# Performance work log

Hardware: AMD Instinct MI355X
Metric: run time of the kernel (lower is better)

The kernel has to match this reference:

```python
import jax, jax.numpy as jnp
import numpy as np

N_ATOMS = 3
HIDDEN = 256
N_PAIRS = N_ATOMS * (N_ATOMS - 1) // 2  # 3
BATCH = 500000


def setup_inputs() -> dict:
    key = jax.random.key(0)
    ks = jax.random.split(key, 8)
    s1 = 1.0 / np.sqrt(N_PAIRS)
    s2 = 1.0 / np.sqrt(HIDDEN)
    return {
        "x": jax.random.normal(ks[0], (BATCH, N_ATOMS * 3), dtype=jnp.float32),
        "W1": jax.random.normal(ks[1], (N_PAIRS, HIDDEN), dtype=jnp.float32) * s1,
        "b1": jnp.zeros((HIDDEN,), dtype=jnp.float32),
        "W2": jax.random.normal(ks[2], (HIDDEN, HIDDEN), dtype=jnp.float32) * s2,
        "b2": jnp.zeros((HIDDEN,), dtype=jnp.float32),
        "W3": jax.random.normal(ks[3], (HIDDEN, 3), dtype=jnp.float32) * s2,
        "b3": jnp.zeros((3,), dtype=jnp.float32),
    }


def reference(x, W1, b1, W2, b2, W3, b3):
    # --- pairwise bond lengths (vectorized over batch) ---
    pts = x.reshape(-1, N_ATOMS, 3)                       # [B, n_atoms, 3]
    iu, ju = np.triu_indices(N_ATOMS, 1)                  # static index arrays
    diff = pts[:, iu, :] - pts[:, ju, :]                  # [B, n_pairs, 3]
    r = jnp.sqrt(jnp.sum(diff * diff, axis=-1))           # [B, n_pairs]
    # --- MLP: Dense->relu->Dense->relu->Dense (sizes=[256,256,3]) ---
    h = jax.nn.relu(r @ W1 + b1)                          # [B, 256]
    h = jax.nn.relu(h @ W2 + b2)                          # [B, 256]
    w = h @ W3 + b3                                       # [B, 3] -> (w00, w11, w01)
    # --- analytic eigenvalues of symmetric 2x2 [[w00,w01],[w01,w11]] ---
    # eigh returns ascending order: mean -/+ radius
    m = 0.5 * (w[:, 0] + w[:, 1])
    d = 0.5 * (w[:, 0] - w[:, 1])
    rad = jnp.sqrt(d * d + w[:, 2] * w[:, 2])
    return jnp.stack([m - rad, m + rad], axis=-1)         # [B, 2]
```

## Files before the change

### kernel.cpp

```cpp
#include <hip/hip_runtime.h>
#include <hip/hip_bf16.h>
#include <stdint.h>

typedef __attribute__((ext_vector_type(8))) short short8;
typedef __attribute__((ext_vector_type(4))) float f32x4;

#define NCHUNK 15625
#define NBLK 256
#define NTHR 512
#define NWAVE_TOT (NBLK * 8)

__device__ __forceinline__ unsigned short f2bf(float f) {
    unsigned int u = __float_as_uint(f);
    u = (u + 0x7fffu + ((u >> 16) & 1u)) >> 16;
    return (unsigned short)u;
}

__global__ void prep_kernel(const float* __restrict__ W1, const float* __restrict__ b1,
                            const float* __restrict__ W2, const float* __restrict__ b2,
                            const float* __restrict__ W3,
                            uint4* __restrict__ w2p, float4* __restrict__ w1b1,
                            float4* __restrict__ w3b2) {
    int id = blockIdx.x * 256 + threadIdx.x;
    if (id < 8192) {
        int lane = id & 63;
        int f = id >> 6;
        int s = f >> 4, t = f & 15;
        int g = lane >> 4, c = lane & 15;
        int n = t * 16 + c;
        int kbase = s * 32 + g * 8;
        unsigned int w[4];
#pragma unroll
        for (int jj = 0; jj < 4; ++jj) {
            unsigned int lo = f2bf(W2[(kbase + 2 * jj) * 256 + n]);
            unsigned int hi = f2bf(W2[(kbase + 2 * jj + 1) * 256 + n]);
            w[jj] = lo | (hi << 16);
        }
        w2p[id] = make_uint4(w[0], w[1], w[2], w[3]);
    } else if (id < 8448) {
        int k = id - 8192;
        w1b1[k] = make_float4(W1[k], W1[256 + k], W1[512 + k], b1[k]);
    } else if (id < 8704) {
        int c2 = id - 8448;
        w3b2[c2] = make_float4(W3[c2 * 3 + 0], W3[c2 * 3 + 1], W3[c2 * 3 + 2], b2[c2]);
    }
}

__global__ __launch_bounds__(NTHR, 2) void fused_kernel(
    const float* __restrict__ x, const uint4* __restrict__ w2p,
    const float4* __restrict__ w1b1, const float4* __restrict__ w3b2,
    const float* __restrict__ b3, float* __restrict__ out)
{
    extern __shared__ char smem[];
    const int tid = threadIdx.x;
    const int lane = tid & 63;
    const int g = lane >> 4;
    const int lr = lane & 15;

    {
        uint4* ls = (uint4*)smem;
#pragma unroll
        for (int it = 0; it < 16; ++it) {
            int idx = it * NTHR + tid;
            ls[idx] = w2p[idx];
        }
    }
    __syncthreads();

    const float b30 = b3[0], b31 = b3[1], b32 = b3[2];
    const short8* bfr = (const short8*)smem;
    const int gwave = blockIdx.x * 8 + (tid >> 6);

    for (int chunk = gwave; chunk < NCHUNK; chunk += NWAVE_TOT) {
        const int row0 = chunk * 32;

        float q0[2], q1[2], q2[2];
#pragma unroll
        for (int mt = 0; mt < 2; ++mt) {
            const float* xp = x + (long)(row0 + mt * 16 + lr) * 9;
            float d0 = xp[0] - xp[3], d1 = xp[1] - xp[4], d2 = xp[2] - xp[5];
            float e0 = xp[0] - xp[6], e1 = xp[1] - xp[7], e2 = xp[2] - xp[8];
            float f0 = xp[3] - xp[6], f1 = xp[4] - xp[7], f2 = xp[5] - xp[8];
            q0[mt] = sqrtf(d0 * d0 + d1 * d1 + d2 * d2);
            q1[mt] = sqrtf(e0 * e0 + e1 * e1 + e2 * e2);
            q2[mt] = sqrtf(f0 * f0 + f1 * f1 + f2 * f2);
        }

        f32x4 acc[2][16];
        const f32x4 zz = {0.0f, 0.0f, 0.0f, 0.0f};
#pragma unroll
        for (int t = 0; t < 16; ++t) { acc[0][t] = zz; acc[1][t] = zz; }

#pragma unroll 1
        for (int s = 0; s < 8; ++s) {
            short8 a0v, a1v;
#pragma unroll
            for (int j = 0; j < 8; ++j) {
                float4 wb = w1b1[s * 32 + g * 8 + j];
                float h0 = fmaf(q0[0], wb.x, fmaf(q1[0], wb.y, fmaf(q2[0], wb.z, wb.w)));
                float h1 = fmaf(q0[1], wb.x, fmaf(q1[1], wb.y, fmaf(q2[1], wb.z, wb.w)));
                a0v[j] = (short)f2bf(fmaxf(h0, 0.0f));
                a1v[j] = (short)f2bf(fmaxf(h1, 0.0f));
            }
#pragma unroll
            for (int t = 0; t < 16; ++t) {
                short8 bv = bfr[(s * 16 + t) * 64 + lane];
                acc[0][t] = __builtin_amdgcn_mfma_f32_16x16x32_bf16(a0v, bv, acc[0][t], 0, 0, 0);
                acc[1][t] = __builtin_amdgcn_mfma_f32_16x16x32_bf16(a1v, bv, acc[1][t], 0, 0, 0);
            }
        }

        float p[2][4][3];
#pragma unroll
        for (int mt = 0; mt < 2; ++mt)
#pragma unroll
            for (int r = 0; r < 4; ++r) { p[mt][r][0] = 0.f; p[mt][r][1] = 0.f; p[mt][r][2] = 0.f; }

#pragma unroll
        for (int t = 0; t < 16; ++t) {
            float4 wb = w3b2[t * 16 + lr];
#pragma unroll
            for (int mt = 0; mt < 2; ++mt)
#pragma unroll
                for (int r = 0; r < 4; ++r) {
                    float v = fmaxf(acc[mt][t][r] + wb.w, 0.0f);
                    p[mt][r][0] = fmaf(v, wb.x, p[mt][r][0]);
                    p[mt][r][1] = fmaf(v, wb.y, p[mt][r][1]);
                    p[mt][r][2] = fmaf(v, wb.z, p[mt][r][2]);
                }
        }

#pragma unroll
        for (int mt = 0; mt < 2; ++mt)
#pragma unroll
            for (int r = 0; r < 4; ++r)
#pragma unroll
                for (int m = 0; m < 3; ++m) {
                    float v = p[mt][r][m];
                    v += __shfl_xor(v, 1, 16);
                    v += __shfl_xor(v, 2, 16);
                    v += __shfl_xor(v, 4, 16);
                    v += __shfl_xor(v, 8, 16);
                    p[mt][r][m] = v;
                }

        if (lr == 0) {
#pragma unroll
            for (int mt = 0; mt < 2; ++mt)
#pragma unroll
                for (int r = 0; r < 4; ++r) {
                    float w0 = p[mt][r][0] + b30;
                    float w1v = p[mt][r][1] + b31;
                    float w2v = p[mt][r][2] + b32;
                    float mm = 0.5f * (w0 + w1v);
                    float dd = 0.5f * (w0 - w1v);
                    float rad = sqrtf(fmaf(dd, dd, w2v * w2v));
                    int row = row0 + mt * 16 + g * 4 + r;
                    float2 o = make_float2(mm - rad, mm + rad);
                    *(float2*)(out + (long)row * 2) = o;
                }
        }
    }
}

extern "C" void kernel_launch(void* const* d_in, const int* in_sizes, int n_in,
                              void* d_out, int out_size, void* d_ws, size_t ws_size,
                              hipStream_t stream) {
    const float* x  = (const float*)d_in[0];
    const float* W1 = (const float*)d_in[1];
    const float* b1 = (const float*)d_in[2];
    const float* W2 = (const float*)d_in[3];
    const float* b2 = (const float*)d_in[4];
    const float* W3 = (const float*)d_in[5];
    const float* b3 = (const float*)d_in[6];
    float* out = (float*)d_out;

    char* ws = (char*)d_ws;
    uint4*  w2p  = (uint4*)ws;
    float4* w1b1 = (float4*)(ws + 131072);
    float4* w3b2 = (float4*)(ws + 135168);

    (void)hipFuncSetAttribute((const void*)fused_kernel,
                              hipFuncAttributeMaxDynamicSharedMemorySize, 131072);

    prep_kernel<<<34, 256, 0, stream>>>(W1, b1, W2, b2, W3, w2p, w1b1, w3b2);
    fused_kernel<<<NBLK, NTHR, 131072, stream>>>(x, w2p, w1b1, w3b2, b3, out);
}
```

Measured before the change: 161.7 us.

## Fuse weight prep into main kernel, transpose GEMM, use MFMA for output layer

Removes the separate prep kernel; each block now loads W2 through an LDS scratch and converts it to bf16 MFMA fragments itself, using the hardware packed bf16 convert instruction. The layer-2 GEMM is transposed so W2 fragments act as the A operand and activations as B, and each wave now handles 64 rows with bias b2 preloaded into the accumulators. The third layer becomes a bf16 MFMA against register-held W3 fragments instead of FMAs plus cross-lane shuffle reductions. The trade-offs are one block per CU with a larger LDS footprint, redundant W2 conversion in every block, and more accumulator registers.

```diff
diff --git a/kernel.cpp b/kernel.cpp
--- a/kernel.cpp
+++ b/kernel.cpp
@@ -5,160 +5,168 @@
 typedef __attribute__((ext_vector_type(8))) short short8;
 typedef __attribute__((ext_vector_type(4))) float f32x4;
 
-#define NCHUNK 15625
+#define NTILE 31250
+#define NCHUNK 7813
 #define NBLK 256
 #define NTHR 512
 #define NWAVE_TOT (NBLK * 8)
 
-__device__ __forceinline__ unsigned short f2bf(float f) {
-    unsigned int u = __float_as_uint(f);
-    u = (u + 0x7fffu + ((u >> 16) & 1u)) >> 16;
-    return (unsigned short)u;
+#define FRAG_OFF   0
+#define W1_OFF     131072
+#define SCR_OFF    135168
+#define LDS_TOTAL  151552
+
+__device__ __forceinline__ uint32_t cvtpk(float lo, float hi) {
+    uint32_t r;
+    asm("v_cvt_pk_bf16_f32 %0, %1, %2" : "=v"(r) : "v"(lo), "v"(hi));
+    return r;
 }
 
-__global__ void prep_kernel(const float* __restrict__ W1, const float* __restrict__ b1,
-                            const float* __restrict__ W2, const float* __restrict__ b2,
-                            const float* __restrict__ W3,
-                            uint4* __restrict__ w2p, float4* __restrict__ w1b1,
-                            float4* __restrict__ w3b2) {
-    int id = blockIdx.x * 256 + threadIdx.x;
-    if (id < 8192) {
-        int lane = id & 63;
-        int f = id >> 6;
-        int s = f >> 4, t = f & 15;
-        int g = lane >> 4, c = lane & 15;
-        int n = t * 16 + c;
-        int kbase = s * 32 + g * 8;
-        unsigned int w[4];
-#pragma unroll
-        for (int jj = 0; jj < 4; ++jj) {
-            unsigned int lo = f2bf(W2[(kbase + 2 * jj) * 256 + n]);
-            unsigned int hi = f2bf(W2[(kbase + 2 * jj + 1) * 256 + n]);
-            w[jj] = lo | (hi << 16);
-        }
-        w2p[id] = make_uint4(w[0], w[1], w[2], w[3]);
-    } else if (id < 8448) {
-        int k = id - 8192;
-        w1b1[k] = make_float4(W1[k], W1[256 + k], W1[512 + k], b1[k]);
-    } else if (id < 8704) {
-        int c2 = id - 8448;
-        w3b2[c2] = make_float4(W3[c2 * 3 + 0], W3[c2 * 3 + 1], W3[c2 * 3 + 2], b2[c2]);
-    }
+__device__ __forceinline__ int sig2(int mp) {
+    int t = mp >> 4, gm = (mp >> 2) & 3, r = mp & 3;
+    return ((t >> 1) << 5) + (gm << 3) + ((t & 1) << 2) + r;
 }
 
-__global__ __launch_bounds__(NTHR, 2) void fused_kernel(
-    const float* __restrict__ x, const uint4* __restrict__ w2p,
-    const float4* __restrict__ w1b1, const float4* __restrict__ w3b2,
+__global__ __launch_bounds__(NTHR, 1) void fused_kernel(
+    const float* __restrict__ x,  const float* __restrict__ W1,
+    const float* __restrict__ b1, const float* __restrict__ W2,
+    const float* __restrict__ b2, const float* __restrict__ W3,
     const float* __restrict__ b3, float* __restrict__ out)
 {
     extern __shared__ char smem[];
-    const int tid = threadIdx.x;
+    uint4*  frag4 = (uint4*)(smem + FRAG_OFF);
+    float4* w1lds = (float4*)(smem + W1_OFF);
+    float*  scrf  = (float*)(smem + SCR_OFF);
+    uint4*  scr4  = (uint4*)(smem + SCR_OFF);
+
+    const int tid  = threadIdx.x;
     const int lane = tid & 63;
-    const int g = lane >> 4;
-    const int lr = lane & 15;
+    const int g    = lane >> 4;
+    const int lr   = lane & 15;
 
-    {
-        uint4* ls = (uint4*)smem;
+    if (tid < 256)
+        w1lds[tid] = make_float4(W1[tid], W1[256 + tid], W1[512 + tid], b1[tid]);
+
+    const uint4* gw2 = (const uint4*)W2;
+    for (int p = 0; p < 16; ++p) {
+        __syncthreads();
+        scr4[tid]       = gw2[p * 1024 + tid];
+        scr4[tid + 512] = gw2[p * 1024 + 512 + tid];
+        __syncthreads();
+        int t   = tid >> 5;
+        int l   = (tid & 31) + ((p & 1) << 5);
+        int c16 = l & 15;
+        int s   = p >> 1;
+        int c   = sig2(t * 16 + c16);
+        int rowbase = ((l >> 4) & 1) * 8;
+        float f[8];
 #pragma unroll
-        for (int it = 0; it < 16; ++it) {
-            int idx = it * NTHR + tid;
-            ls[idx] = w2p[idx];
-        }
+        for (int j = 0; j < 8; ++j) f[j] = scrf[(rowbase + j) * 256 + c];
+        uint4 wv;
+        wv.x = cvtpk(f[0], f[1]); wv.y = cvtpk(f[2], f[3]);
+        wv.z = cvtpk(f[4], f[5]); wv.w = cvtpk(f[6], f[7]);
+        frag4[(s * 16 + t) * 64 + l] = wv;
     }
     __syncthreads();
 
+    float4 b2v[16];
+#pragma unroll
+    for (int t = 0; t < 16; ++t) {
+        int bc = ((t >> 1) << 5) + (g << 3) + ((t & 1) << 2);
+        b2v[t] = *(const float4*)(b2 + bc);
+    }
+    short8 w3f[8];
+#pragma unroll
+    for (int s2 = 0; s2 < 8; ++s2) {
+        float f3[8];
+#pragma unroll
+        for (int j = 0; j < 8; ++j) {
+            int kk = s2 * 32 + g * 8 + j;
+            f3[j] = (lr < 3) ? W3[kk * 3 + lr] : 0.0f;
+        }
+        union { short8 s8; uint32_t u[4]; } pw;
+        pw.u[0] = cvtpk(f3[0], f3[1]); pw.u[1] = cvtpk(f3[2], f3[3]);
+        pw.u[2] = cvtpk(f3[4], f3[5]); pw.u[3] = cvtpk(f3[6], f3[7]);
+        w3f[s2] = pw.s8;
+    }
     const float b30 = b3[0], b31 = b3[1], b32 = b3[2];
-    const short8* bfr = (const short8*)smem;
+
+    const short8* afr = (const short8*)(smem + FRAG_OFF);
     const int gwave = blockIdx.x * 8 + (tid >> 6);
 
     for (int chunk = gwave; chunk < NCHUNK; chunk += NWAVE_TOT) {
-        const int row0 = chunk * 32;
+        const int row0 = chunk * 64;
 
-        float q0[2], q1[2], q2[2];
+        float q0[4], q1[4], q2[4];
 #pragma unroll
-        for (int mt = 0; mt < 2; ++mt) {
-            const float* xp = x + (long)(row0 + mt * 16 + lr) * 9;
-            float d0 = xp[0] - xp[3], d1 = xp[1] - xp[4], d2 = xp[2] - xp[5];
-            float e0 = xp[0] - xp[6], e1 = xp[1] - xp[7], e2 = xp[2] - xp[8];
-            float f0 = xp[3] - xp[6], f1 = xp[4] - xp[7], f2 = xp[5] - xp[8];
-            q0[mt] = sqrtf(d0 * d0 + d1 * d1 + d2 * d2);
-            q1[mt] = sqrtf(e0 * e0 + e1 * e1 + e2 * e2);
-            q2[mt] = sqrtf(f0 * f0 + f1 * f1 + f2 * f2);
+        for (int nt = 0; nt < 4; ++nt) {
+            if (chunk * 4 + nt < NTILE) {
+                const float* xp = x + (size_t)(row0 + nt * 16 + lr) * 9;
+                float a0 = xp[0], a1 = xp[1], a2 = xp[2], a3 = xp[3], a4 = xp[4];
+                float a5 = xp[5], a6 = xp[6], a7 = xp[7], a8 = xp[8];
+                float d0 = a0 - a3, d1 = a1 - a4, d2 = a2 - a5;
+                float e0 = a0 - a6, e1 = a1 - a7, e2 = a2 - a8;
+                float f0 = a3 - a6, f1 = a4 - a7, f2 = a5 - a8;
+                q0[nt] = sqrtf(fmaf(d0, d0, fmaf(d1, d1, d2 * d2)));
+                q1[nt] = sqrtf(fmaf(e0, e0, fmaf(e1, e1, e2 * e2)));
+                q2[nt] = sqrtf(fmaf(f0, f0, fmaf(f1, f1, f2 * f2)));
+            } else { q0[nt] = 1.f; q1[nt] = 1.f; q2[nt] = 1.f; }
         }
 
-        f32x4 acc[2][16];
-        const f32x4 zz = {0.0f, 0.0f, 0.0f, 0.0f};
+        f32x4 acc[16][4];
 #pragma unroll
-        for (int t = 0; t < 16; ++t) { acc[0][t] = zz; acc[1][t] = zz; }
+        for (int t = 0; t < 16; ++t) {
+            f32x4 bi; bi[0] = b2v[t].x; bi[1] = b2v[t].y; bi[2] = b2v[t].z; bi[3] = b2v[t].w;
+#pragma unroll
+            for (int nt = 0; nt < 4; ++nt) acc[t][nt] = bi;
+        }
 
 #pragma unroll 1
         for (int s = 0; s < 8; ++s) {
-            short8 a0v, a1v;
+            float4 wv[8];
 #pragma unroll
-            for (int j = 0; j < 8; ++j) {
-                float4 wb = w1b1[s * 32 + g * 8 + j];
-                float h0 = fmaf(q0[0], wb.x, fmaf(q1[0], wb.y, fmaf(q2[0], wb.z, wb.w)));
-                float h1 = fmaf(q0[1], wb.x, fmaf(q1[1], wb.y, fmaf(q2[1], wb.z, wb.w)));
-                a0v[j] = (short)f2bf(fmaxf(h0, 0.0f));
-                a1v[j] = (short)f2bf(fmaxf(h1, 0.0f));
+            for (int j = 0; j < 8; ++j) wv[j] = w1lds[s * 32 + g * 8 + j];
+            short8 hb[4];
+#pragma unroll
+            for (int nt = 0; nt < 4; ++nt) {
+                union { short8 s8; uint32_t u[4]; } pk;
+#pragma unroll
+                for (int jj = 0; jj < 4; ++jj) {
+                    float4 wa = wv[2 * jj], wb = wv[2 * jj + 1];
+                    float ha = fmaf(q0[nt], wa.x, fmaf(q1[nt], wa.y, fmaf(q2[nt], wa.z, wa.w)));
+                    float hc = fmaf(q0[nt], wb.x, fmaf(q1[nt], wb.y, fmaf(q2[nt], wb.z, wb.w)));
+                    pk.u[jj] = cvtpk(fmaxf(ha, 0.f), fmaxf(hc, 0.f));
+                }
+                hb[nt] = pk.s8;
             }
 #pragma unroll
             for (int t = 0; t < 16; ++t) {
-                short8 bv = bfr[(s * 16 + t) * 64 + lane];
-                acc[0][t] = __builtin_amdgcn_mfma_f32_16x16x32_bf16(a0v, bv, acc[0][t], 0, 0, 0);
-                acc[1][t] = __builtin_amdgcn_mfma_f32_16x16x32_bf16(a1v, bv, acc[1][t], 0, 0, 0);
+                short8 av = afr[(s * 16 + t) * 64 + lane];
+#pragma unroll
+                for (int nt = 0; nt < 4; ++nt)
+                    acc[t][nt] = __builtin_amdgcn_mfma_f32_16x16x32_bf16(av, hb[nt], acc[t][nt], 0, 0, 0);
             }
         }
 
-        float p[2][4][3];
 #pragma unroll
-        for (int mt = 0; mt < 2; ++mt)
+        for (int nt = 0; nt < 4; ++nt) {
+            f32x4 D = {0.f, 0.f, 0.f, 0.f};
 #pragma unroll
-            for (int r = 0; r < 4; ++r) { p[mt][r][0] = 0.f; p[mt][r][1] = 0.f; p[mt][r][2] = 0.f; }
-
-#pragma unroll
-        for (int t = 0; t < 16; ++t) {
-            float4 wb = w3b2[t * 16 + lr];
-#pragma unroll
-            for (int mt = 0; mt < 2; ++mt)
-#pragma unroll
-                for (int r = 0; r < 4; ++r) {
-                    float v = fmaxf(acc[mt][t][r] + wb.w, 0.0f);
-                    p[mt][r][0] = fmaf(v, wb.x, p[mt][r][0]);
-                    p[mt][r][1] = fmaf(v, wb.y, p[mt][r][1]);
-                    p[mt][r][2] = fmaf(v, wb.z, p[mt][r][2]);
-                }
-        }
-
-#pragma unroll
-        for (int mt = 0; mt < 2; ++mt)
-#pragma unroll
-            for (int r = 0; r < 4; ++r)
-#pragma unroll
-                for (int m = 0; m < 3; ++m) {
-                    float v = p[mt][r][m];
-                    v += __shfl_xor(v, 1, 16);
-                    v += __shfl_xor(v, 2, 16);
-                    v += __shfl_xor(v, 4, 16);
-                    v += __shfl_xor(v, 8, 16);
-                    p[mt][r][m] = v;
-                }
-
-        if (lr == 0) {
-#pragma unroll
-            for (int mt = 0; mt < 2; ++mt)
-#pragma unroll
-                for (int r = 0; r < 4; ++r) {
-                    float w0 = p[mt][r][0] + b30;
-                    float w1v = p[mt][r][1] + b31;
-                    float w2v = p[mt][r][2] + b32;
-                    float mm = 0.5f * (w0 + w1v);
-                    float dd = 0.5f * (w0 - w1v);
-                    float rad = sqrtf(fmaf(dd, dd, w2v * w2v));
-                    int row = row0 + mt * 16 + g * 4 + r;
-                    float2 o = make_float2(mm - rad, mm + rad);
-                    *(float2*)(out + (long)row * 2) = o;
-                }
+            for (int s2 = 0; s2 < 8; ++s2) {
+                union { short8 s8; uint32_t u[4]; } pb;
+                pb.u[0] = cvtpk(fmaxf(acc[2 * s2][nt][0], 0.f), fmaxf(acc[2 * s2][nt][1], 0.f));
+                pb.u[1] = cvtpk(fmaxf(acc[2 * s2][nt][2], 0.f), fmaxf(acc[2 * s2][nt][3], 0.f));
+                pb.u[2] = cvtpk(fmaxf(acc[2 * s2 + 1][nt][0], 0.f), fmaxf(acc[2 * s2 + 1][nt][1], 0.f));
+                pb.u[3] = cvtpk(fmaxf(acc[2 * s2 + 1][nt][2], 0.f), fmaxf(acc[2 * s2 + 1][nt][3], 0.f));
+                D = __builtin_amdgcn_mfma_f32_16x16x32_bf16(w3f[s2], pb.s8, D, 0, 0, 0);
+            }
+            if (g == 0 && (chunk * 4 + nt) < NTILE) {
+                float w0 = D[0] + b30, w1v = D[1] + b31, wc = D[2] + b32;
+                float mm = 0.5f * (w0 + w1v), dd = 0.5f * (w0 - w1v);
+                float rad = sqrtf(fmaf(dd, dd, wc * wc));
+                int row = row0 + nt * 16 + lr;
+                *(float2*)(out + (size_t)row * 2) = make_float2(mm - rad, mm + rad);
+            }
         }
     }
 }
@@ -175,14 +183,10 @@
     const float* b3 = (const float*)d_in[6];
     float* out = (float*)d_out;
 
-    char* ws = (char*)d_ws;
-    uint4*  w2p  = (uint4*)ws;
-    float4* w1b1 = (float4*)(ws + 131072);
-    float4* w3b2 = (float4*)(ws + 135168);
+    (void)d_ws; (void)ws_size;
 
     (void)hipFuncSetAttribute((const void*)fused_kernel,
-                              hipFuncAttributeMaxDynamicSharedMemorySize, 131072);
+                              hipFuncAttributeMaxDynamicSharedMemorySize, LDS_TOTAL);
 
-    prep_kernel<<<34, 256, 0, stream>>>(W1, b1, W2, b2, W3, w2p, w1b1, w3b2);
-    fused_kernel<<<NBLK, NTHR, 131072, stream>>>(x, w2p, w1b1, w3b2, b3, out);
+    fused_kernel<<<NBLK, NTHR, LDS_TOTAL, stream>>>(x, W1, b1, W2, b2, W3, b3, out);
 }
```

New measurement: 406.5 us. 2.51x slower.
